# Kernel optimization log

Hardware: AMD Instinct MI355X
Metric: run time of the kernel (lower is better)

Reference implementation:

```python
import jax, jax.numpy as jnp
import numpy as np


def setup_inputs() -> dict:
    key = jax.random.key(0)
    k1, k2, k3, k4 = jax.random.split(key, 4)
    n1, n2, d, num_types = 8192, 8192, 512, 64
    return {
        "input1": jax.random.normal(k1, (n1, d), dtype=jnp.float32),
        "input2": jax.random.normal(k2, (n2, d), dtype=jnp.float32),
        "weight": jax.random.normal(k3, (num_types, d), dtype=jnp.float32),
        "bias": jax.random.uniform(k4, (1,), dtype=jnp.float32),
        "type_index": 3,
    }


def reference(input1, input2, weight, bias, type_index):
    # DistMult score: (input1 * w_r) @ input2^T + bias.
    # Original builds diag(w_r) and does a dense d x d GEMM; the faithful
    # math is an elementwise row-scale followed by one GEMM.
    w_r = weight[type_index]                      # [d]
    scaled = input1 * w_r[None, :]                # [n1, d]
    out = scaled @ input2.T + bias                # [n1, n2]
    return out  # act is identity
```

## Files before the change

### kernel.cpp

```cpp
#include <hip/hip_runtime.h>


#define N1 8192
#define N2 8192
#define DK 512
#define BM 128
#define BN 128
#define BK 32

typedef short bf16x8 __attribute__((ext_vector_type(8)));
typedef float f32x4 __attribute__((ext_vector_type(4)));

__device__ __forceinline__ unsigned short f2bf(float f) {
    unsigned int u = __float_as_uint(f);
    u = (u + 0x7FFFu + ((u >> 16) & 1u)) >> 16;
    return (unsigned short)u;
}

__global__ __launch_bounds__(256) void convert_kernel(
        const float* __restrict__ in1, const float* __restrict__ in2,
        const float* __restrict__ weight, const int* __restrict__ type_index,
        unsigned short* __restrict__ a_bf, unsigned short* __restrict__ b_bf) {
    const int QA = N1 * DK / 4;
    int i = blockIdx.x * blockDim.x + threadIdx.x;
    if (i < QA) {
        float4 v = reinterpret_cast<const float4*>(in1)[i];
        int c4 = i & (DK / 4 - 1);
        float4 w = reinterpret_cast<const float4*>(weight + (size_t)(*type_index) * DK)[c4];
        ushort4 o;
        o.x = f2bf(v.x * w.x);
        o.y = f2bf(v.y * w.y);
        o.z = f2bf(v.z * w.z);
        o.w = f2bf(v.w * w.w);
        reinterpret_cast<ushort4*>(a_bf)[i] = o;
    } else {
        int j = i - QA;
        float4 v = reinterpret_cast<const float4*>(in2)[j];
        ushort4 o;
        o.x = f2bf(v.x);
        o.y = f2bf(v.y);
        o.z = f2bf(v.z);
        o.w = f2bf(v.w);
        reinterpret_cast<ushort4*>(b_bf)[j] = o;
    }
}

__global__ __launch_bounds__(256) void gemm_bt(
        const unsigned short* __restrict__ A, const unsigned short* __restrict__ B,
        const float* __restrict__ bias, float* __restrict__ C) {
    __shared__ __align__(16) unsigned short ldsA[BM * BK];
    __shared__ __align__(16) unsigned short ldsB[BN * BK];

    const int tid  = threadIdx.x;
    const int wave = tid >> 6;
    const int lane = tid & 63;
    const int quad = lane >> 4;
    const int r16  = lane & 15;
    const int wm   = wave & 1;
    const int wn   = wave >> 1;

    const int bm = blockIdx.y * BM;
    const int bn = blockIdx.x * BN;

    f32x4 acc[4][4];
#pragma unroll
    for (int i = 0; i < 4; ++i)
#pragma unroll
        for (int j = 0; j < 4; ++j)
            acc[i][j] = (f32x4){0.f, 0.f, 0.f, 0.f};

    const int srow = wave * 32 + (lane >> 2);
    const int scol = (lane & 3) * 8;
    const unsigned short* ag0 = A + (size_t)(bm + srow) * DK + scol;
    const unsigned short* ag1 = ag0 + 16 * DK;
    const unsigned short* bg0 = B + (size_t)(bn + srow) * DK + scol;
    const unsigned short* bg1 = bg0 + 16 * DK;

    unsigned short* la0 = &ldsA[wave * 1024];
    unsigned short* la1 = &ldsA[wave * 1024 + 512];
    unsigned short* lb0 = &ldsB[wave * 1024];
    unsigned short* lb1 = &ldsB[wave * 1024 + 512];

    for (int kt = 0; kt < DK; kt += BK) {
        __builtin_amdgcn_global_load_lds(ag0 + kt, la0, 16, 0, 0);
        __builtin_amdgcn_global_load_lds(ag1 + kt, la1, 16, 0, 0);
        __builtin_amdgcn_global_load_lds(bg0 + kt, lb0, 16, 0, 0);
        __builtin_amdgcn_global_load_lds(bg1 + kt, lb1, 16, 0, 0);
        __syncthreads();

        bf16x8 af[4], bfr[4];
#pragma unroll
        for (int mi = 0; mi < 4; ++mi)
            af[mi] = *(const bf16x8*)&ldsA[(wm * 64 + mi * 16 + r16) * BK + quad * 8];
#pragma unroll
        for (int ni = 0; ni < 4; ++ni)
            bfr[ni] = *(const bf16x8*)&ldsB[(wn * 64 + ni * 16 + r16) * BK + quad * 8];

#pragma unroll
        for (int mi = 0; mi < 4; ++mi)
#pragma unroll
            for (int ni = 0; ni < 4; ++ni)
                acc[mi][ni] = __builtin_amdgcn_mfma_f32_16x16x32_bf16(
                    af[mi], bfr[ni], acc[mi][ni], 0, 0, 0);
        __syncthreads();
    }

    const float bv = bias[0];
#pragma unroll
    for (int mi = 0; mi < 4; ++mi) {
        const int row0 = bm + wm * 64 + mi * 16 + quad * 4;
#pragma unroll
        for (int ni = 0; ni < 4; ++ni) {
            const int col = bn + wn * 64 + ni * 16 + r16;
#pragma unroll
            for (int r = 0; r < 4; ++r)
                C[(size_t)(row0 + r) * N2 + col] = acc[mi][ni][r] + bv;
        }
    }
}

__global__ void naive_kernel(const float* __restrict__ in1, const float* __restrict__ in2,
                             const float* __restrict__ weight, const int* __restrict__ type_index,
                             const float* __restrict__ bias, float* __restrict__ out) {
    int col = blockIdx.x * 16 + threadIdx.x;
    int row = blockIdx.y * 16 + threadIdx.y;
    const float* wr = weight + (size_t)(*type_index) * DK;
    float s = 0.f;
    for (int k = 0; k < DK; ++k)
        s += in1[(size_t)row * DK + k] * wr[k] * in2[(size_t)col * DK + k];
    out[(size_t)row * N2 + col] = s + bias[0];
}

extern "C" void kernel_launch(void* const* d_in, const int* in_sizes, int n_in,
                              void* d_out, int out_size, void* d_ws, size_t ws_size,
                              hipStream_t stream) {
    const float* in1  = (const float*)d_in[0];
    const float* in2  = (const float*)d_in[1];
    const float* wgt  = (const float*)d_in[2];
    const float* bias = (const float*)d_in[3];
    const int*   tix  = (const int*)d_in[4];
    float* out = (float*)d_out;

    const size_t need = 2ull * (N1 + N2) * DK;
    if (ws_size >= need) {
        unsigned short* a_bf = (unsigned short*)d_ws;
        unsigned short* b_bf = a_bf + (size_t)N1 * DK;

        const int total4 = (N1 + N2) * DK / 4;
        convert_kernel<<<total4 / 256, 256, 0, stream>>>(in1, in2, wgt, tix, a_bf, b_bf);

        dim3 grid(N2 / BN, N1 / BM);
        gemm_bt<<<grid, 256, 0, stream>>>(a_bf, b_bf, bias, out);
    } else {
        dim3 grid(N2 / 16, N1 / 16);
        dim3 blk(16, 16);
        naive_kernel<<<grid, blk, 0, stream>>>(in1, in2, wgt, tix, bias, out);
    }
}
```

Measured before the change: 353.1 us.

## Double K tile to 64 and swizzle blocks across XCDs for L2 reuse

Raises the GEMM K-tile from 32 to 64. Each wave now issues four wider direct-to-LDS loads per operand and runs two MFMA substeps per barrier pair, which halves the number of synchronizations. The launch becomes a 1D grid, and block IDs are remapped so each XCD handles a contiguous band of output column tiles. This is meant to improve L2 reuse of the B operand. LDS usage doubles, and the longer row stride may change bank-conflict patterns.

```diff
diff --git a/kernel.cpp b/kernel.cpp
--- a/kernel.cpp
+++ b/kernel.cpp
@@ -6,7 +6,7 @@
 #define DK 512
 #define BM 128
 #define BN 128
-#define BK 32
+#define BK 64
 
 typedef short bf16x8 __attribute__((ext_vector_type(8)));
 typedef float f32x4 __attribute__((ext_vector_type(4)));
@@ -59,8 +59,13 @@
     const int wm   = wave & 1;
     const int wn   = wave >> 1;
 
-    const int bm = blockIdx.y * BM;
-    const int bn = blockIdx.x * BN;
+    const int bid   = blockIdx.x;
+    const int xcd   = bid & 7;
+    const int inner = bid >> 3;
+    const int tn    = xcd * 8 + (inner & 7);
+    const int tm    = inner >> 3;
+    const int bm = tm * BM;
+    const int bn = tn * BN;
 
     f32x4 acc[4][4];
 #pragma unroll
@@ -69,39 +74,38 @@
         for (int j = 0; j < 4; ++j)
             acc[i][j] = (f32x4){0.f, 0.f, 0.f, 0.f};
 
-    const int srow = wave * 32 + (lane >> 2);
-    const int scol = (lane & 3) * 8;
-    const unsigned short* ag0 = A + (size_t)(bm + srow) * DK + scol;
-    const unsigned short* ag1 = ag0 + 16 * DK;
-    const unsigned short* bg0 = B + (size_t)(bn + srow) * DK + scol;
-    const unsigned short* bg1 = bg0 + 16 * DK;
-
-    unsigned short* la0 = &ldsA[wave * 1024];
-    unsigned short* la1 = &ldsA[wave * 1024 + 512];
-    unsigned short* lb0 = &ldsB[wave * 1024];
-    unsigned short* lb1 = &ldsB[wave * 1024 + 512];
+    const int srow = wave * 32 + (lane >> 3);
+    const int scol = (lane & 7) * 8;
+    const unsigned short* ag = A + (size_t)(bm + srow) * DK + scol;
+    const unsigned short* bg = B + (size_t)(bn + srow) * DK + scol;
+    unsigned short* la = &ldsA[wave * 32 * BK];
+    unsigned short* lb = &ldsB[wave * 32 * BK];
 
     for (int kt = 0; kt < DK; kt += BK) {
-        __builtin_amdgcn_global_load_lds(ag0 + kt, la0, 16, 0, 0);
-        __builtin_amdgcn_global_load_lds(ag1 + kt, la1, 16, 0, 0);
-        __builtin_amdgcn_global_load_lds(bg0 + kt, lb0, 16, 0, 0);
-        __builtin_amdgcn_global_load_lds(bg1 + kt, lb1, 16, 0, 0);
+#pragma unroll
+        for (int c = 0; c < 4; ++c) {
+            __builtin_amdgcn_global_load_lds(ag + kt + (size_t)(c * 8) * DK, la + c * 8 * BK, 16, 0, 0);
+            __builtin_amdgcn_global_load_lds(bg + kt + (size_t)(c * 8) * DK, lb + c * 8 * BK, 16, 0, 0);
+        }
         __syncthreads();
 
-        bf16x8 af[4], bfr[4];
 #pragma unroll
-        for (int mi = 0; mi < 4; ++mi)
-            af[mi] = *(const bf16x8*)&ldsA[(wm * 64 + mi * 16 + r16) * BK + quad * 8];
+        for (int ks = 0; ks < 2; ++ks) {
+            bf16x8 af[4], bfr[4];
 #pragma unroll
-        for (int ni = 0; ni < 4; ++ni)
-            bfr[ni] = *(const bf16x8*)&ldsB[(wn * 64 + ni * 16 + r16) * BK + quad * 8];
+            for (int mi = 0; mi < 4; ++mi)
+                af[mi] = *(const bf16x8*)&ldsA[(wm * 64 + mi * 16 + r16) * BK + ks * 32 + quad * 8];
+#pragma unroll
+            for (int ni = 0; ni < 4; ++ni)
+                bfr[ni] = *(const bf16x8*)&ldsB[(wn * 64 + ni * 16 + r16) * BK + ks * 32 + quad * 8];
 
 #pragma unroll
-        for (int mi = 0; mi < 4; ++mi)
+            for (int mi = 0; mi < 4; ++mi)
 #pragma unroll
-            for (int ni = 0; ni < 4; ++ni)
-                acc[mi][ni] = __builtin_amdgcn_mfma_f32_16x16x32_bf16(
-                    af[mi], bfr[ni], acc[mi][ni], 0, 0, 0);
+                for (int ni = 0; ni < 4; ++ni)
+                    acc[mi][ni] = __builtin_amdgcn_mfma_f32_16x16x32_bf16(
+                        af[mi], bfr[ni], acc[mi][ni], 0, 0, 0);
+        }
         __syncthreads();
     }
 
@@ -149,8 +153,7 @@
         const int total4 = (N1 + N2) * DK / 4;
         convert_kernel<<<total4 / 256, 256, 0, stream>>>(in1, in2, wgt, tix, a_bf, b_bf);
 
-        dim3 grid(N2 / BN, N1 / BM);
-        gemm_bt<<<grid, 256, 0, stream>>>(a_bf, b_bf, bias, out);
+        gemm_bt<<<(N1 / BM) * (N2 / BN), 256, 0, stream>>>(a_bf, b_bf, bias, out);
     } else {
         dim3 grid(N2 / 16, N1 / 16);
         dim3 blk(16, 16);
```

Measured after the change: 364.1 us. +3.1%, slower.
